# Optimization experiments

Hardware: AMD Instinct MI355X
Metric: run time of the kernel (lower is better)

Reference implementation:

```python
import jax, jax.numpy as jnp
import numpy as np
from jax.ops import segment_sum

N_NODES = 50000
N_EDGES = 800000
NUM_FEAT = 16
EDGE_DIM = 8
H = 100
L = 2
BN_EPS = 1e-5


def setup_inputs() -> dict:
    key = jax.random.key(0)
    ks = iter(jax.random.split(key, 40))
    def w(shape, scale=0.05):
        return (jax.random.normal(next(ks), shape, dtype=jnp.float32) * scale)
    inp = {
        "x": jax.random.normal(next(ks), (N_NODES, NUM_FEAT), dtype=jnp.float32),
        "edge_index": jax.random.randint(next(ks), (2, N_EDGES), 0, N_NODES, dtype=jnp.int64) if jax.config.jax_enable_x64 else jax.random.randint(next(ks), (2, N_EDGES), 0, N_NODES).astype(jnp.int32),
        "edge_attr": jax.random.normal(next(ks), (N_EDGES, EDGE_DIM), dtype=jnp.float32),
        # embeddings
        "node_w": w((NUM_FEAT, H)), "node_b": w((H,)),
        "edge_w": w((EDGE_DIM, H)), "edge_b": w((H,)),
        # per-layer GINEConv MLP (stacked over layers)
        "conv_w1": w((L, H, H)), "conv_b1": w((L, H)),
        "conv_w2": w((L, H, H)), "conv_b2": w((L, H)),
        # batchnorm affine params
        "bn_gamma": jnp.ones((L, H), dtype=jnp.float32), "bn_beta": jnp.zeros((L, H), dtype=jnp.float32),
        # per-layer edge-update MLP
        "emlp_w1": w((L, 3 * H, H)), "emlp_b1": w((L, H)),
        "emlp_w2": w((L, H, H)), "emlp_b2": w((L, H)),
        # final classifier MLP (3H -> 50 -> 25 -> 2); dropout is identity at eval
        "mlp_w1": w((3 * H, 50)), "mlp_b1": w((50,)),
        "mlp_w2": w((50, 25)), "mlp_b2": w((25,)),
        "mlp_w3": w((25, 2)), "mlp_b3": w((2,)),
    }
    return inp


def reference(x, edge_index, edge_attr,
              node_w, node_b, edge_w, edge_b,
              conv_w1, conv_b1, conv_w2, conv_b2,
              bn_gamma, bn_beta,
              emlp_w1, emlp_b1, emlp_w2, emlp_b2,
              mlp_w1, mlp_b1, mlp_w2, mlp_b2, mlp_w3, mlp_b3):
    src, dst = edge_index[0], edge_index[1]
    n_nodes = x.shape[0]

    h = x @ node_w + node_b          # [N, H]
    e = edge_attr @ edge_w + edge_b  # [E, H]

    for i in range(L):
        # GINEConv: out_i = nn((1+eps)*h_i + sum_{e: dst=i} relu(h_src + e)); eps=0
        msg = jax.nn.relu(h[src] + e)                       # [E, H] gather + combine
        agg = segment_sum(msg, dst, num_segments=n_nodes)   # [N, H] scatter-add
        z = h + agg
        z = jax.nn.relu(z @ conv_w1[i] + conv_b1[i]) @ conv_w2[i] + conv_b2[i]
        # BatchNorm (train mode: batch stats over nodes, biased variance)
        mu = jnp.mean(z, axis=0)
        var = jnp.var(z, axis=0)
        z = (z - mu) * jax.lax.rsqrt(var + BN_EPS) * bn_gamma[i] + bn_beta[i]
        h = (h + jax.nn.relu(z)) * 0.5
        # edge update: e += MLP([h_src, h_dst, e]) / 2
        cat = jnp.concatenate([h[src], h[dst], e], axis=-1)  # [E, 3H]
        upd = jax.nn.relu(cat @ emlp_w1[i] + emlp_b1[i]) @ emlp_w2[i] + emlp_b2[i]
        e = e + upd * 0.5

    # per-edge features: relu([h_src, h_dst]) ++ e  -> [E, 3H]
    feat = jnp.concatenate([jax.nn.relu(jnp.concatenate([h[src], h[dst]], axis=-1)), e], axis=-1)
    out = jax.nn.relu(feat @ mlp_w1 + mlp_b1)
    out = jax.nn.relu(out @ mlp_w2 + mlp_b2)
    return out @ mlp_w3 + mlp_b3  # [E, 2]
```

## Files before the change

### kernel.cpp

```cpp
#include <hip/hip_runtime.h>
#include <hip/hip_bf16.h>

#define N_NODES 50000
#define N_EDGES 800000
#define HDIM 100
#define ESTR 104

typedef _Float16 half8_t __attribute__((ext_vector_type(8)));
typedef _Float16 half4_t __attribute__((ext_vector_type(4)));
typedef float f32x4_t __attribute__((ext_vector_type(4)));

struct FragDesc {
  const float* src; int stride; int K; int N; int outOff; int ksteps; int ntiles;
};
struct PrepArgs {
  FragDesc d[20];
  int prefix[21];
  int ndesc;
};

__global__ void k_prep_frags(PrepArgs args, _Float16* __restrict__ out) {
  int b = blockIdx.x;
  int di = 0;
  while (di + 1 < args.ndesc && b >= args.prefix[di + 1]) di++;
  FragDesc d = args.d[di];
  int local = b - args.prefix[di];
  int t = local / d.ksteps;
  int s = local % d.ksteps;
  int lane = threadIdx.x;
  int col = t * 16 + (lane & 15);
  int kb = s * 32 + (lane >> 4) * 8;
  _Float16* o = out + d.outOff + (size_t)((t * d.ksteps + s) * 64 + lane) * 8;
  #pragma unroll
  for (int i = 0; i < 8; ++i) {
    int k = kb + i;
    float v = (k < d.K && col < d.N) ? d.src[(size_t)k * d.stride + col] : 0.0f;
    o[i] = (_Float16)v;
  }
}

__global__ void k_ws_probe(float* out, float mb) { out[0] = mb; }

__device__ __forceinline__ half8_t h8_zero() {
  half8_t a;
  #pragma unroll
  for (int i = 0; i < 8; ++i) a[i] = (_Float16)0.0f;
  return a;
}

__device__ __forceinline__ int swz_idx(int r, int c) {
  int chunk = (c >> 3) ^ (r & 7);
  return r * 128 + chunk * 8 + (c & 7);
}

template<int MODE>
__device__ __forceinline__ void load_a_node(const float* hp0,
                                            const float* ap0,
                                            int row, int lane, half8_t av[4]) {
  int g = lane >> 4;
  bool rv = (row < N_NODES);
  const float* hp = hp0 + (size_t)row * HDIM;
  const float* ap = ap0 + (size_t)row * HDIM;
  #pragma unroll
  for (int s = 0; s < 4; ++s) {
    int kb = s * 32 + g * 8;
    half8_t a = h8_zero();
    if (rv && kb < HDIM) {
      float f[8];
      #pragma unroll
      for (int i = 0; i < 8; ++i) f[i] = 0.0f;
      if (kb + 8 <= HDIM) {
        float4 v0 = *(const float4*)(hp + kb);
        float4 v1 = *(const float4*)(hp + kb + 4);
        f[0] = v0.x; f[1] = v0.y; f[2] = v0.z; f[3] = v0.w;
        f[4] = v1.x; f[5] = v1.y; f[6] = v1.z; f[7] = v1.w;
        if constexpr (MODE == 2) {
          float4 u0 = *(const float4*)(ap + kb);
          float4 u1 = *(const float4*)(ap + kb + 4);
          f[0] += u0.x; f[1] += u0.y; f[2] += u0.z; f[3] += u0.w;
          f[4] += u1.x; f[5] += u1.y; f[6] += u1.z; f[7] += u1.w;
        }
      } else {
        float4 v0 = *(const float4*)(hp + kb);
        f[0] = v0.x; f[1] = v0.y; f[2] = v0.z; f[3] = v0.w;
        if constexpr (MODE == 2) {
          float4 u0 = *(const float4*)(ap + kb);
          f[0] += u0.x; f[1] += u0.y; f[2] += u0.z; f[3] += u0.w;
        }
      }
      #pragma unroll
      for (int i = 0; i < 8; ++i) {
        float v = f[i];
        if constexpr (MODE == 1) v = fmaxf(v, 0.0f);
        a[i] = (_Float16)v;
      }
    }
    av[s] = a;
  }
}

template<int NT, int KS>
__device__ __forceinline__ void mfma_tiles(const half8_t* av, const _Float16* __restrict__ fb,
                                           int lane, f32x4_t* acc) {
  #pragma unroll
  for (int t = 0; t < NT; ++t) {
    #pragma unroll
    for (int s = 0; s < KS; ++s) {
      half8_t bv = *(const half8_t*)(fb + (size_t)(((t * KS + s) * 64 + lane) << 3));
      acc[t] = __builtin_amdgcn_mfma_f32_16x16x32_f16(av[s], bv, acc[t], 0, 0, 0);
    }
  }
}

template<int KS>
__device__ __forceinline__ void lds_read_a(const _Float16* L, int lane, half8_t* av) {
  int r = lane & 15;
  int g = lane >> 4;
  #pragma unroll
  for (int s = 0; s < KS; ++s) {
    int kb = s * 32 + g * 8;
    av[s] = *(const half8_t*)&L[swz_idx(r, kb)];
  }
}

__global__ void k_embed_h(const float* __restrict__ x, const float* __restrict__ w,
                          const float* __restrict__ bias, float* __restrict__ h) {
  int n = blockIdx.x;
  int j = threadIdx.x;
  if (j >= HDIM) return;
  float acc = bias[j];
  #pragma unroll
  for (int k = 0; k < 16; ++k) acc += x[n * 16 + k] * w[k * HDIM + j];
  h[(size_t)n * HDIM + j] = acc;
}

__global__ void k_embed_e(const float* __restrict__ attr, const float* __restrict__ w,
                          const float* __restrict__ bias, const int* __restrict__ src,
                          const int* __restrict__ dst, const float* __restrict__ h,
                          _Float16* __restrict__ e, float* __restrict__ agg) {
  int tid = threadIdx.x;
  int edge = blockIdx.x * 2 + (tid >> 7);
  int j = tid & 127;
  if (edge >= N_EDGES || j >= ESTR) return;
  float acc = 0.0f;
  if (j < HDIM) {
    acc = bias[j];
    #pragma unroll
    for (int k = 0; k < 8; ++k) acc += attr[(size_t)edge * 8 + k] * w[k * HDIM + j];
  }
  e[(size_t)edge * ESTR + j] = (_Float16)acc;
  if (j < HDIM) {
    float m = h[(size_t)src[edge] * HDIM + j] + acc;
    if (m > 0.0f) atomicAdd(&agg[(size_t)dst[edge] * HDIM + j], m);
  }
}

__global__ __launch_bounds__(256) void k_node_conv(
    const float* __restrict__ h, const float* agg,
    const _Float16* __restrict__ fb1, const _Float16* __restrict__ fb2,
    const float* __restrict__ b1, const float* __restrict__ b2,
    float* z, float* __restrict__ bn_sum, float* __restrict__ bn_sq) {
  __shared__ __align__(16) _Float16 lds[4][2048];
  int lane = threadIdx.x & 63;
  int wave = threadIdx.x >> 6;
  _Float16* L = lds[wave];
  int mbase = (blockIdx.x * 4 + wave) * 16;

  half8_t av[4];
  load_a_node<2>(h, agg, mbase + (lane & 15), lane, av);
  f32x4_t acc[7];
  #pragma unroll
  for (int t = 0; t < 7; ++t) acc[t] = (f32x4_t){0.f, 0.f, 0.f, 0.f};
  mfma_tiles<7, 4>(av, fb1, lane, acc);

  #pragma unroll
  for (int t = 0; t < 7; ++t) {
    int j = t * 16 + (lane & 15);
    float bias = (j < HDIM) ? b1[j] : 0.0f;
    #pragma unroll
    for (int q = 0; q < 4; ++q) {
      int r = (lane >> 4) * 4 + q;
      float v = fmaxf(acc[t][q] + bias, 0.0f);
      if (j >= HDIM) v = 0.0f;
      L[swz_idx(r, j)] = (_Float16)v;
    }
  }
  {
    int r = lane >> 2; int c0 = 112 + (lane & 3) * 4;
    #pragma unroll
    for (int i = 0; i < 4; ++i) L[swz_idx(r, c0 + i)] = (_Float16)0.0f;
  }
  __builtin_amdgcn_sched_barrier(0);

  half8_t av2[4];
  lds_read_a<4>(L, lane, av2);
  f32x4_t acc2[7];
  #pragma unroll
  for (int t = 0; t < 7; ++t) acc2[t] = (f32x4_t){0.f, 0.f, 0.f, 0.f};
  mfma_tiles<7, 4>(av2, fb2, lane, acc2);
  __builtin_amdgcn_sched_barrier(0);

  #pragma unroll
  for (int t = 0; t < 7; ++t) {
    int j = t * 16 + (lane & 15);
    float bias = (j < HDIM) ? b2[j] : 0.0f;
    float colsum = 0.0f, colsq = 0.0f;
    #pragma unroll
    for (int q = 0; q < 4; ++q) {
      int row = mbase + (lane >> 4) * 4 + q;
      float v = acc2[t][q] + bias;
      bool ok = (row < N_NODES) && (j < HDIM);
      if (ok) z[(size_t)row * HDIM + j] = v;
      float sv = ok ? v : 0.0f;
      colsum += sv; colsq += sv * sv;
    }
    colsum += __shfl_xor(colsum, 16);
    colsum += __shfl_xor(colsum, 32);
    colsq  += __shfl_xor(colsq, 16);
    colsq  += __shfl_xor(colsq, 32);
    if (lane < 16 && j < HDIM) {
      atomicAdd(&bn_sum[j], colsum);
      atomicAdd(&bn_sq[j], colsq);
    }
  }
}

__global__ void k_bn_final(const float* __restrict__ bn_sum, const float* __restrict__ bn_sq,
                           float* __restrict__ bn_mu, float* __restrict__ bn_rs) {
  int j = threadIdx.x;
  if (j >= HDIM) return;
  float mu = bn_sum[j] / (float)N_NODES;
  float var = bn_sq[j] / (float)N_NODES - mu * mu;
  bn_mu[j] = mu;
  bn_rs[j] = rsqrtf(var + 1e-5f);
}

__global__ void k_h_update(float* __restrict__ h, const float* __restrict__ z,
                           const float* __restrict__ bn_mu, const float* __restrict__ bn_rs,
                           const float* __restrict__ gamma, const float* __restrict__ beta) {
  int idx = blockIdx.x * blockDim.x + threadIdx.x;
  if (idx >= N_NODES * HDIM) return;
  int j = idx % HDIM;
  float zn = (z[idx] - bn_mu[j]) * bn_rs[j] * gamma[j] + beta[j];
  h[idx] = 0.5f * (h[idx] + fmaxf(zn, 0.0f));
}

template<bool RS>
__global__ __launch_bounds__(256) void k_node_gemm_t(const float* __restrict__ h,
                                                     const _Float16* __restrict__ fb,
                                                     _Float16* __restrict__ out) {
  constexpr int NT = RS ? 8 : 14;
  int lane = threadIdx.x & 63;
  int wave = threadIdx.x >> 6;
  int c = lane & 15;
  int mbase = (blockIdx.x * 4 + wave) * 16;
  half8_t av[4];
  load_a_node<RS ? 1 : 0>(h, h, mbase + c, lane, av);
  f32x4_t acc[NT];
  #pragma unroll
  for (int t = 0; t < NT; ++t) acc[t] = (f32x4_t){0.f, 0.f, 0.f, 0.f};
  mfma_tiles<NT, 4>(av, fb, lane, acc);
  #pragma unroll
  for (int q = 0; q < 4; ++q) {
    int row = mbase + (lane >> 4) * 4 + q;
    if (row >= N_NODES) continue;
    if constexpr (!RS) {
      half8_t hp, hq;
      #pragma unroll
      for (int t = 0; t < 8; ++t) {
        hp[t] = (t < 7) ? (_Float16)acc[t][q] : (_Float16)0.0f;
        hq[t] = (t < 7) ? (_Float16)acc[7 + t][q] : (_Float16)0.0f;
      }
      *(half8_t*)(out + (size_t)row * 256 + c * 8) = hp;
      *(half8_t*)(out + (size_t)row * 256 + 128 + c * 8) = hq;
    } else {
      half4_t hr, hs;
      #pragma unroll
      for (int t = 0; t < 4; ++t) {
        hr[t] = (_Float16)acc[t][q];
        hs[t] = (_Float16)acc[4 + t][q];
      }
      *(half4_t*)(out + (size_t)row * 128 + c * 4) = hr;
      *(half4_t*)(out + (size_t)row * 128 + 64 + c * 4) = hs;
    }
  }
}

template<bool CLASSIFY>
__global__ __launch_bounds__(256) void k_edge(
    _Float16* __restrict__ e, const float* __restrict__ h,
    const _Float16* __restrict__ PQ,
    const int* __restrict__ src, const int* __restrict__ dst,
    const _Float16* __restrict__ fbW1c, const _Float16* __restrict__ fbW2,
    const float* __restrict__ b1, const float* __restrict__ b2,
    float* __restrict__ agg,
    const _Float16* __restrict__ RS,
    const _Float16* __restrict__ fbC, const _Float16* __restrict__ fbM2,
    const _Float16* __restrict__ fbM3,
    const float* __restrict__ mb1, const float* __restrict__ mb2,
    const float* __restrict__ mb3,
    float* __restrict__ out) {
  __shared__ __align__(16) _Float16 lds[4][2048];
  int lane = threadIdx.x & 63;
  int wave = threadIdx.x >> 6;
  _Float16* L = lds[wave];
  int mbase = (blockIdx.x * 4 + wave) * 16;
  int c = lane & 15, g = lane >> 4;

  int sn[4], dn[4];
  #pragma unroll
  for (int q = 0; q < 4; ++q) {
    int row = mbase + g * 4 + q;
    sn[q] = src[row]; dn[q] = dst[row];
  }

  half8_t Pf[4], Qf[4];
  #pragma unroll
  for (int q = 0; q < 4; ++q) {
    Pf[q] = *(const half8_t*)(PQ + (size_t)sn[q] * 256 + c * 8);
    Qf[q] = *(const half8_t*)(PQ + (size_t)dn[q] * 256 + 128 + c * 8);
  }

  half8_t av[4];
  {
    const _Float16* ep = e + (size_t)(mbase + c) * ESTR;
    #pragma unroll
    for (int s = 0; s < 3; ++s)
      av[s] = *(const half8_t*)(ep + s * 32 + g * 8);
    av[3] = (g == 0) ? *(const half8_t*)(ep + 96) : h8_zero();
  }
  f32x4_t acc[7];
  #pragma unroll
  for (int t = 0; t < 7; ++t) acc[t] = (f32x4_t){0.f, 0.f, 0.f, 0.f};
  mfma_tiles<7, 4>(av, fbW1c, lane, acc);

  #pragma unroll
  for (int t = 0; t < 7; ++t) {
    int j = t * 16 + c;
    float bias = (j < HDIM) ? b1[j] : 0.0f;
    #pragma unroll
    for (int q = 0; q < 4; ++q) {
      int r = g * 4 + q;
      float v = 0.0f;
      if (j < HDIM)
        v = fmaxf(acc[t][q] + bias + (float)Pf[q][t] + (float)Qf[q][t], 0.0f);
      L[swz_idx(r, j)] = (_Float16)v;
    }
  }
  { int r = lane >> 2; int c0 = 112 + (lane & 3) * 4;
    #pragma unroll
    for (int i = 0; i < 4; ++i) L[swz_idx(r, c0 + i)] = (_Float16)0.0f;
  }
  __builtin_amdgcn_sched_barrier(0);

  half4_t Rf[4], Sf[4];
  if constexpr (CLASSIFY) {
    #pragma unroll
    for (int q = 0; q < 4; ++q) {
      Rf[q] = *(const half4_t*)(RS + (size_t)sn[q] * 128 + c * 4);
      Sf[q] = *(const half4_t*)(RS + (size_t)dn[q] * 128 + 64 + c * 4);
    }
  }

  half8_t av2[4];
  lds_read_a<4>(L, lane, av2);
  f32x4_t acc2[7];
  #pragma unroll
  for (int t = 0; t < 7; ++t) acc2[t] = (f32x4_t){0.f, 0.f, 0.f, 0.f};
  mfma_tiles<7, 4>(av2, fbW2, lane, acc2);
  __builtin_amdgcn_sched_barrier(0);

  #pragma unroll
  for (int t = 0; t < 7; ++t) {
    int j = t * 16 + c;
    float bias = (j < HDIM) ? b2[j] : 0.0f;
    #pragma unroll
    for (int q = 0; q < 4; ++q) {
      int row = mbase + g * 4 + q;
      float upd = acc2[t][q] + bias;
      float enew = 0.0f;
      if (j < HDIM) {
        float eold = (float)e[(size_t)row * ESTR + j];
        enew = eold + 0.5f * upd;
      }
      if constexpr (!CLASSIFY) {
        if (j < HDIM) {
          e[(size_t)row * ESTR + j] = (_Float16)enew;
          float m = h[(size_t)sn[q] * HDIM + j] + enew;
          if (m > 0.0f) atomicAdd(&agg[(size_t)dn[q] * HDIM + j], m);
        }
      } else {
        int r = g * 4 + q;
        L[swz_idx(r, j)] = (_Float16)((j < HDIM) ? enew : 0.0f);
      }
    }
  }

  if constexpr (CLASSIFY) {
    __builtin_amdgcn_sched_barrier(0);
    half8_t av3[4];
    lds_read_a<4>(L, lane, av3);
    f32x4_t acc3[4];
    #pragma unroll
    for (int t = 0; t < 4; ++t) acc3[t] = (f32x4_t){0.f, 0.f, 0.f, 0.f};
    mfma_tiles<4, 4>(av3, fbC, lane, acc3);
    __builtin_amdgcn_sched_barrier(0);
    #pragma unroll
    for (int t = 0; t < 4; ++t) {
      int j = t * 16 + c;
      float bias = (j < 50) ? mb1[j] : 0.0f;
      #pragma unroll
      for (int q = 0; q < 4; ++q) {
        float v = 0.0f;
        if (j < 50)
          v = fmaxf(acc3[t][q] + bias + (float)Rf[q][t] + (float)Sf[q][t], 0.0f);
        int r = g * 4 + q;
        L[swz_idx(r, j)] = (_Float16)v;
      }
    }
    __builtin_amdgcn_sched_barrier(0);
    half8_t av4[2];
    lds_read_a<2>(L, lane, av4);
    f32x4_t acc4[2];
    #pragma unroll
    for (int t = 0; t < 2; ++t) acc4[t] = (f32x4_t){0.f, 0.f, 0.f, 0.f};
    mfma_tiles<2, 2>(av4, fbM2, lane, acc4);
    __builtin_amdgcn_sched_barrier(0);
    #pragma unroll
    for (int t = 0; t < 2; ++t) {
      int j = t * 16 + c;
      float bias = (j < 25) ? mb2[j] : 0.0f;
      #pragma unroll
      for (int q = 0; q < 4; ++q) {
        float v = (j < 25) ? fmaxf(acc4[t][q] + bias, 0.0f) : 0.0f;
        int r = g * 4 + q;
        L[swz_idx(r, j)] = (_Float16)v;
      }
    }
    __builtin_amdgcn_sched_barrier(0);
    half8_t av5[1];
    lds_read_a<1>(L, lane, av5);
    f32x4_t acc5 = (f32x4_t){0.f, 0.f, 0.f, 0.f};
    {
      half8_t bv = *(const half8_t*)(fbM3 + (size_t)(lane << 3));
      acc5 = __builtin_amdgcn_mfma_f32_16x16x32_f16(av5[0], bv, acc5, 0, 0, 0);
    }
    if (c < 2) {
      float bias = mb3[c];
      #pragma unroll
      for (int q = 0; q < 4; ++q) {
        int row = mbase + g * 4 + q;
        out[(size_t)row * 2 + c] = acc5[q] + bias;
      }
    }
  }
}

extern "C" void kernel_launch(void* const* d_in, const int* in_sizes, int n_in,
                              void* d_out, int out_size, void* d_ws, size_t ws_size,
                              hipStream_t stream) {
  const float* x        = (const float*)d_in[0];
  const int*   ei       = (const int*)  d_in[1];
  const float* eattr    = (const float*)d_in[2];
  const float* node_w   = (const float*)d_in[3];
  const float* node_b   = (const float*)d_in[4];
  const float* edge_w   = (const float*)d_in[5];
  const float* edge_b   = (const float*)d_in[6];
  const float* conv_w1  = (const float*)d_in[7];
  const float* conv_b1  = (const float*)d_in[8];
  const float* conv_w2  = (const float*)d_in[9];
  const float* conv_b2  = (const float*)d_in[10];
  const float* bn_gamma = (const float*)d_in[11];
  const float* bn_beta  = (const float*)d_in[12];
  const float* emlp_w1  = (const float*)d_in[13];
  const float* emlp_b1  = (const float*)d_in[14];
  const float* emlp_w2  = (const float*)d_in[15];
  const float* emlp_b2  = (const float*)d_in[16];
  const float* mlp_w1   = (const float*)d_in[17];
  const float* mlp_b1   = (const float*)d_in[18];
  const float* mlp_w2   = (const float*)d_in[19];
  const float* mlp_b2   = (const float*)d_in[20];
  const float* mlp_w3   = (const float*)d_in[21];
  const float* mlp_b3   = (const float*)d_in[22];
  const int* src = ei;
  const int* dst = ei + N_EDGES;

  char* ws = (char*)d_ws;
  size_t off = 0;
  auto alloc = [&](size_t bytes) -> void* {
    void* p = ws + off;
    off += (bytes + 255) & ~(size_t)255;
    return p;
  };
  _Float16* e    = (_Float16*)alloc((size_t)N_EDGES * ESTR * 2);
  float* h       = (float*)alloc((size_t)N_NODES * HDIM * 4);
  float* agg     = (float*)alloc((size_t)N_NODES * HDIM * 4);
  _Float16* PQt  = (_Float16*)alloc((size_t)N_NODES * 256 * 2);
  float* bn_sum  = (float*)alloc(512);
  float* bn_sq   = (float*)alloc(512);
  float* bn_mu   = (float*)alloc(512);
  float* bn_rs   = (float*)alloc(512);
  _Float16* frags = (_Float16*)alloc(200000 * 2);
  float* z = agg;
  _Float16* RSt = (_Float16*)agg;

  if (off > ws_size) {
    k_ws_probe<<<1, 1, 0, stream>>>((float*)d_out, (float)(ws_size >> 20));
    return;
  }

  PrepArgs pa;
  int nd = 0, tilesum = 0, fo = 0;
  auto add = [&](const float* sp, int stride, int K, int Ncols, int ksteps, int ntiles) -> int {
    pa.d[nd] = FragDesc{sp, stride, K, Ncols, fo, ksteps, ntiles};
    pa.prefix[nd] = tilesum;
    tilesum += ksteps * ntiles;
    ++nd;
    int ret = fo;
    fo += ksteps * ntiles * 512;
    return ret;
  };
  int offConvW1[2], offConvW2[2], offPQ[2], offW1c[2], offW2e[2];
  for (int i = 0; i < 2; ++i) {
    offConvW1[i] = add(conv_w1 + i * 10000, 100, 100, 100, 4, 7);
    offConvW2[i] = add(conv_w2 + i * 10000, 100, 100, 100, 4, 7);
    offPQ[i]     = add(emlp_w1 + i * 30000,         100, 100, 100, 4, 7);
                   add(emlp_w1 + i * 30000 + 10000, 100, 100, 100, 4, 7);
    offW1c[i]    = add(emlp_w1 + i * 30000 + 20000, 100, 100, 100, 4, 7);
    offW2e[i]    = add(emlp_w2 + i * 10000, 100, 100, 100, 4, 7);
  }
  int offRS = add(mlp_w1,         50, 100, 50, 4, 4);
              add(mlp_w1 + 5000,  50, 100, 50, 4, 4);
  int offC  = add(mlp_w1 + 10000, 50, 100, 50, 4, 4);
  int offM2 = add(mlp_w2, 25, 50, 25, 2, 2);
  int offM3 = add(mlp_w3, 2, 25, 2, 1, 1);
  pa.prefix[nd] = tilesum;
  pa.ndesc = nd;

  const size_t aggBytes = (size_t)N_NODES * HDIM * 4;

  hipMemsetAsync(agg, 0, aggBytes, stream);
  k_prep_frags<<<tilesum, 64, 0, stream>>>(pa, frags);
  k_embed_h<<<N_NODES, 128, 0, stream>>>(x, node_w, node_b, h);
  k_embed_e<<<N_EDGES / 2, 256, 0, stream>>>(eattr, edge_w, edge_b, src, dst, h, e, agg);

  const int nodeGrid = (N_NODES + 63) / 64;
  for (int i = 0; i < 2; ++i) {
    hipMemsetAsync(bn_sum, 0, 512, stream);
    hipMemsetAsync(bn_sq, 0, 512, stream);
    k_node_conv<<<nodeGrid, 256, 0, stream>>>(h, agg, frags + offConvW1[i], frags + offConvW2[i],
                                              conv_b1 + i * 100, conv_b2 + i * 100,
                                              z, bn_sum, bn_sq);
    k_bn_final<<<1, 128, 0, stream>>>(bn_sum, bn_sq, bn_mu, bn_rs);
    k_h_update<<<(N_NODES * HDIM + 255) / 256, 256, 0, stream>>>(h, z, bn_mu, bn_rs,
                                                                 bn_gamma + i * 100, bn_beta + i * 100);
    k_node_gemm_t<false><<<nodeGrid, 256, 0, stream>>>(h, frags + offPQ[i], PQt);
    if (i == 0) {
      hipMemsetAsync(agg, 0, aggBytes, stream);
      k_edge<false><<<N_EDGES / 64, 256, 0, stream>>>(
          e, h, PQt, src, dst, frags + offW1c[0], frags + offW2e[0],
          emlp_b1, emlp_b2, agg,
          nullptr, nullptr, nullptr, nullptr, nullptr, nullptr, nullptr, nullptr);
    } else {
      k_node_gemm_t<true><<<nodeGrid, 256, 0, stream>>>(h, frags + offRS, RSt);
      k_edge<true><<<N_EDGES / 64, 256, 0, stream>>>(
          e, h, PQt, src, dst, frags + offW1c[1], frags + offW2e[1],
          emlp_b1 + 100, emlp_b2 + 100, nullptr,
          RSt, frags + offC, frags + offM2, frags + offM3,
          mlp_b1, mlp_b2, mlp_b3, (float*)d_out);
    }
  }
}
```

Baseline: 1.688 ms.

## Replace atomic scatter-add aggregation with CSR gather-based segment sum

Builds a dst-sorted CSR on every call (histogram, single-block scan, atomic permutation) and computes each node's aggregation by gathering its incoming edges, replacing per-edge float atomicAdd scatter in the embedding and edge kernels. This removes atomic contention and the memsets of agg, and recomputes the layer-0 edge embedding inside the gather. In exchange it adds three preprocessing kernels, including a serial 1024-thread scan, plus indirect, uncoalesced reads of e rows through perm. Edge order within a segment is nondeterministic, so results can vary slightly in float summation order.

```diff
diff --git a/kernel.cpp b/kernel.cpp
--- a/kernel.cpp
+++ b/kernel.cpp
@@ -40,6 +40,93 @@
 }
 
 __global__ void k_ws_probe(float* out, float mb) { out[0] = mb; }
+
+__global__ void k_hist(const int* __restrict__ dst, int* __restrict__ cnt) {
+  for (int e = blockIdx.x * blockDim.x + threadIdx.x; e < N_EDGES;
+       e += gridDim.x * blockDim.x)
+    atomicAdd(&cnt[dst[e]], 1);
+}
+
+__global__ __launch_bounds__(1024) void k_scan(const int* __restrict__ cnt,
+                                               int* __restrict__ rowptr,
+                                               int* __restrict__ cursor) {
+  __shared__ int part[1024];
+  int t = threadIdx.x;
+  const int CH = (N_NODES + 1023) / 1024;
+  int base = t * CH;
+  int s = 0;
+  for (int i = 0; i < CH; ++i) {
+    int n = base + i;
+    if (n < N_NODES) s += cnt[n];
+  }
+  part[t] = s;
+  __syncthreads();
+  for (int off = 1; off < 1024; off <<= 1) {
+    int v = 0;
+    if (t >= off) v = part[t - off];
+    __syncthreads();
+    if (t >= off) part[t] += v;
+    __syncthreads();
+  }
+  int run = (t == 0) ? 0 : part[t - 1];
+  for (int i = 0; i < CH; ++i) {
+    int n = base + i;
+    if (n <= N_NODES) {
+      rowptr[n] = run;
+      if (n < N_NODES) { cursor[n] = run; run += cnt[n]; }
+    }
+  }
+}
+
+__global__ void k_perm(const int* __restrict__ src, const int* __restrict__ dst,
+                       int* __restrict__ cursor, int* __restrict__ perm,
+                       int* __restrict__ srcS) {
+  for (int e = blockIdx.x * blockDim.x + threadIdx.x; e < N_EDGES;
+       e += gridDim.x * blockDim.x) {
+    int pos = atomicAdd(&cursor[dst[e]], 1);
+    perm[pos] = e;
+    srcS[pos] = src[e];
+  }
+}
+
+template<bool L0>
+__global__ __launch_bounds__(256) void k_agg(
+    const int* __restrict__ rowptr, const int* __restrict__ perm,
+    const int* __restrict__ srcS,
+    const float* __restrict__ attr, const float* __restrict__ ew,
+    const float* __restrict__ ebias,
+    const _Float16* __restrict__ e,
+    const float* __restrict__ h, float* __restrict__ agg) {
+  __shared__ float EwL[800];
+  __shared__ float ebL[128];
+  int tid = threadIdx.x;
+  if constexpr (L0) {
+    for (int idx = tid; idx < 800; idx += 256) EwL[idx] = ew[idx];
+    if (tid < 128) ebL[tid] = (tid < HDIM) ? ebias[tid] : 0.0f;
+    __syncthreads();
+  }
+  int n = blockIdx.x * 2 + (tid >> 7);
+  int j = tid & 127;
+  if (n >= N_NODES || j >= HDIM) return;
+  float acc = 0.0f;
+  int p0 = rowptr[n], p1 = rowptr[n + 1];
+  for (int pos = p0; pos < p1; ++pos) {
+    int s = srcS[pos];
+    int eid = perm[pos];
+    float m;
+    if constexpr (L0) {
+      const float* ap = attr + (size_t)eid * 8;
+      float e0 = ebL[j];
+      #pragma unroll
+      for (int k = 0; k < 8; ++k) e0 += ap[k] * EwL[k * HDIM + j];
+      m = h[(size_t)s * HDIM + j] + e0;
+    } else {
+      m = h[(size_t)s * HDIM + j] + (float)e[(size_t)eid * ESTR + j];
+    }
+    acc += fmaxf(m, 0.0f);
+  }
+  agg[(size_t)n * HDIM + j] = acc;
+}
 
 __device__ __forceinline__ half8_t h8_zero() {
   half8_t a;
@@ -135,9 +222,8 @@
 }
 
 __global__ void k_embed_e(const float* __restrict__ attr, const float* __restrict__ w,
-                          const float* __restrict__ bias, const int* __restrict__ src,
-                          const int* __restrict__ dst, const float* __restrict__ h,
-                          _Float16* __restrict__ e, float* __restrict__ agg) {
+                          const float* __restrict__ bias,
+                          _Float16* __restrict__ e) {
   int tid = threadIdx.x;
   int edge = blockIdx.x * 2 + (tid >> 7);
   int j = tid & 127;
@@ -149,10 +235,6 @@
     for (int k = 0; k < 8; ++k) acc += attr[(size_t)edge * 8 + k] * w[k * HDIM + j];
   }
   e[(size_t)edge * ESTR + j] = (_Float16)acc;
-  if (j < HDIM) {
-    float m = h[(size_t)src[edge] * HDIM + j] + acc;
-    if (m > 0.0f) atomicAdd(&agg[(size_t)dst[edge] * HDIM + j], m);
-  }
 }
 
 __global__ __launch_bounds__(256) void k_node_conv(
@@ -288,12 +370,11 @@
 
 template<bool CLASSIFY>
 __global__ __launch_bounds__(256) void k_edge(
-    _Float16* __restrict__ e, const float* __restrict__ h,
+    _Float16* __restrict__ e,
     const _Float16* __restrict__ PQ,
     const int* __restrict__ src, const int* __restrict__ dst,
     const _Float16* __restrict__ fbW1c, const _Float16* __restrict__ fbW2,
     const float* __restrict__ b1, const float* __restrict__ b2,
-    float* __restrict__ agg,
     const _Float16* __restrict__ RS,
     const _Float16* __restrict__ fbC, const _Float16* __restrict__ fbM2,
     const _Float16* __restrict__ fbM3,
@@ -384,11 +465,7 @@
         enew = eold + 0.5f * upd;
       }
       if constexpr (!CLASSIFY) {
-        if (j < HDIM) {
-          e[(size_t)row * ESTR + j] = (_Float16)enew;
-          float m = h[(size_t)sn[q] * HDIM + j] + enew;
-          if (m > 0.0f) atomicAdd(&agg[(size_t)dn[q] * HDIM + j], m);
-        }
+        if (j < HDIM) e[(size_t)row * ESTR + j] = (_Float16)enew;
       } else {
         int r = g * 4 + q;
         L[swz_idx(r, j)] = (_Float16)((j < HDIM) ? enew : 0.0f);
@@ -496,6 +573,11 @@
   float* h       = (float*)alloc((size_t)N_NODES * HDIM * 4);
   float* agg     = (float*)alloc((size_t)N_NODES * HDIM * 4);
   _Float16* PQt  = (_Float16*)alloc((size_t)N_NODES * 256 * 2);
+  int* cnt       = (int*)alloc((size_t)N_NODES * 4);
+  int* cursor    = (int*)alloc((size_t)N_NODES * 4);
+  int* rowptr    = (int*)alloc((size_t)(N_NODES + 1) * 4);
+  int* perm      = (int*)alloc((size_t)N_EDGES * 4);
+  int* srcS      = (int*)alloc((size_t)N_EDGES * 4);
   float* bn_sum  = (float*)alloc(512);
   float* bn_sq   = (float*)alloc(512);
   float* bn_mu   = (float*)alloc(512);
@@ -537,12 +619,17 @@
   pa.prefix[nd] = tilesum;
   pa.ndesc = nd;
 
-  const size_t aggBytes = (size_t)N_NODES * HDIM * 4;
-
-  hipMemsetAsync(agg, 0, aggBytes, stream);
+  hipMemsetAsync(cnt, 0, (size_t)N_NODES * 4, stream);
+  k_hist<<<2048, 256, 0, stream>>>(dst, cnt);
+  k_scan<<<1, 1024, 0, stream>>>(cnt, rowptr, cursor);
+  k_perm<<<2048, 256, 0, stream>>>(src, dst, cursor, perm, srcS);
+
   k_prep_frags<<<tilesum, 64, 0, stream>>>(pa, frags);
   k_embed_h<<<N_NODES, 128, 0, stream>>>(x, node_w, node_b, h);
-  k_embed_e<<<N_EDGES / 2, 256, 0, stream>>>(eattr, edge_w, edge_b, src, dst, h, e, agg);
+  k_embed_e<<<N_EDGES / 2, 256, 0, stream>>>(eattr, edge_w, edge_b, e);
+  k_agg<true><<<N_NODES / 2, 256, 0, stream>>>(rowptr, perm, srcS,
+                                               eattr, edge_w, edge_b,
+                                               nullptr, h, agg);
 
   const int nodeGrid = (N_NODES + 63) / 64;
   for (int i = 0; i < 2; ++i) {
@@ -556,16 +643,18 @@
                                                                  bn_gamma + i * 100, bn_beta + i * 100);
     k_node_gemm_t<false><<<nodeGrid, 256, 0, stream>>>(h, frags + offPQ[i], PQt);
     if (i == 0) {
-      hipMemsetAsync(agg, 0, aggBytes, stream);
       k_edge<false><<<N_EDGES / 64, 256, 0, stream>>>(
-          e, h, PQt, src, dst, frags + offW1c[0], frags + offW2e[0],
-          emlp_b1, emlp_b2, agg,
+          e, PQt, src, dst, frags + offW1c[0], frags + offW2e[0],
+          emlp_b1, emlp_b2,
           nullptr, nullptr, nullptr, nullptr, nullptr, nullptr, nullptr, nullptr);
+      k_agg<false><<<N_NODES / 2, 256, 0, stream>>>(rowptr, perm, srcS,
+                                                    nullptr, nullptr, nullptr,
+                                                    e, h, agg);
     } else {
       k_node_gemm_t<true><<<nodeGrid, 256, 0, stream>>>(h, frags + offRS, RSt);
       k_edge<true><<<N_EDGES / 64, 256, 0, stream>>>(
-          e, h, PQt, src, dst, frags + offW1c[1], frags + offW2e[1],
-          emlp_b1 + 100, emlp_b2 + 100, nullptr,
+          e, PQt, src, dst, frags + offW1c[1], frags + offW2e[1],
+          emlp_b1 + 100, emlp_b2 + 100,
           RSt, frags + offC, frags + offM2, frags + offM3,
           mlp_b1, mlp_b2, mlp_b3, (float*)d_out);
     }
```

Result: no change. 1.658 ms (-1.8%).
